# Kernel optimization log

Hardware: AMD Instinct MI355X
Metric: run time of the kernel (lower is better)

Reference implementation:

```python
import jax, jax.numpy as jnp
import numpy as np

NUM_HEADS = 12
HEAD_DIM = 64


def setup_inputs() -> dict:
    key = jax.random.key(0)
    k1, k2, k3 = jax.random.split(key, 3)
    x = jax.random.normal(k1, (64, 768, 14, 14), dtype=jnp.float32)
    # 1x1 conv weights stored as [out_ch, in_ch]; scaled to keep softmax logits sane
    w_qkv = jax.random.normal(k2, (3 * NUM_HEADS * HEAD_DIM, 768), dtype=jnp.float32) * 0.02
    w_proj = jax.random.normal(k3, (768, NUM_HEADS * HEAD_DIM), dtype=jnp.float32) * 0.02
    return {"x": x, "w_qkv": w_qkv, "w_proj": w_proj}


def reference(x, w_qkv, w_proj):
    B, C, H, W = x.shape
    N = H * W
    scale = HEAD_DIM ** -0.25  # qk_scale=None -> head_dim**-0.25, applied to both q and k
    # 1x1 conv == channel matmul: [B,3*nh*dh,H,W]
    qkv = jnp.einsum('oc,bchw->bohw', w_qkv, x)
    # rearrange 'b (x y z) h w -> x b y (h w) z'
    qkv = qkv.reshape(B, 3, NUM_HEADS, HEAD_DIM, N).transpose(1, 0, 2, 4, 3)  # [3,B,nh,N,dh]
    q, k, v = qkv[0], qkv[1], qkv[2]
    attn = jnp.einsum('bhnd,bhmd->bhnm', q * scale, k * scale)  # [B,nh,N,N]
    attn = jax.nn.softmax(attn, axis=-1)
    out = jnp.einsum('bhnm,bhmd->bhnd', attn, v)  # [B,nh,N,dh]
    # rearrange 'b y (h w) z -> b (y z) h w'
    out = out.transpose(0, 1, 3, 2).reshape(B, NUM_HEADS * HEAD_DIM, H, W)
    out = jnp.einsum('oc,bchw->bohw', w_proj, out)  # proj 1x1 conv, no bias
    return out
```

## Files before the change

### kernel.cpp

```cpp
#include <hip/hip_runtime.h>
#include <cstdint>
#include <cstddef>

#define NH     12
#define DH     64
#define CIN    768
#define NPIX   196
#define NB     64
#define ROWS   (NB * NPIX)
#define QKV_OC 2304
#define NKT    12

typedef __attribute__((ext_vector_type(8))) _Float16 f16x8;
typedef __attribute__((ext_vector_type(4))) _Float16 f16x4;
typedef __attribute__((ext_vector_type(4))) float    f32x4;

#define MFMA16 __builtin_amdgcn_mfma_f32_16x16x32_f16

__global__ __launch_bounds__(256) void k_convert_w(const float* __restrict__ wq,
                                                   const float* __restrict__ wp,
                                                   _Float16* __restrict__ out) {
    int i = blockIdx.x * 256 + threadIdx.x;
    const int NQ = QKV_OC * CIN / 4;
    const int NT = NQ + (CIN * CIN) / 4;
    if (i >= NT) return;
    float4 v = (i < NQ) ? ((const float4*)wq)[i] : ((const float4*)wp)[i - NQ];
    f16x4 o = { (_Float16)v.x, (_Float16)v.y, (_Float16)v.z, (_Float16)v.w };
    ((f16x4*)out)[i] = o;
}

__global__ __launch_bounds__(256) void k_transpose_x(const float* __restrict__ x,
                                                     _Float16* __restrict__ Xt) {
    __shared__ __align__(16) _Float16 lds[NPIX][72];
    int t  = threadIdx.x;
    int b  = blockIdx.y, c0 = blockIdx.x * 64;
    const float* xp = x + ((size_t)b * CIN + c0) * NPIX;
    for (int idx = t; idx < 64 * 49; idx += 256) {
        int c = idx / 49, k = idx - c * 49;
        float4 v = *(const float4*)(xp + (size_t)c * NPIX + k * 4);
        int n = k * 4;
        lds[n][c]     = (_Float16)v.x;
        lds[n + 1][c] = (_Float16)v.y;
        lds[n + 2][c] = (_Float16)v.z;
        lds[n + 3][c] = (_Float16)v.w;
    }
    __syncthreads();
    int cs = t & 7, nn = t >> 3;
    for (int n = nn; n < NPIX; n += 32) {
        _Float16* dst = Xt + ((size_t)(b * NPIX + n)) * CIN + c0 + cs * 8;
        *(ulonglong2*)dst = *(const ulonglong2*)&lds[n][cs * 8];
    }
}

__device__ inline void gload16(const _Float16* g, _Float16* l) {
    __builtin_amdgcn_global_load_lds((const __attribute__((address_space(1))) void*)g,
                                     (__attribute__((address_space(3))) void*)l,
                                     16, 0, 0);
}

template<int NTN, bool PROJ>
__global__ __launch_bounds__(512, 2) void k_gemm2(const _Float16* __restrict__ A,
                                                  const _Float16* __restrict__ Bm,
                                                  _Float16* __restrict__ Cb,
                                                  float* __restrict__ Cf) {
    __shared__ __align__(16) _Float16 As[2][256 * 64];
    __shared__ __align__(16) _Float16 Bs[2][256 * 64];
    int tid = threadIdx.x;
    int w = tid >> 6, lane = tid & 63;

    int nwg = gridDim.x;
    int orig = blockIdx.x;
    int q = nwg >> 3, r = nwg & 7;
    int xcd = orig & 7, within = orig >> 3;
    int wg = (xcd < r ? xcd * (q + 1) : r * (q + 1) + (xcd - r) * q) + within;
    int bm = wg / NTN, bn = wg - bm * NTN;
    int m0 = bm * 256, n0 = bn * 256;

    int wr = w >> 2, wc = w & 3;
    int r16 = lane & 15, q4 = lane >> 4;

    int sr8  = (w << 3) + (lane >> 3);
    int swz8 = ((lane & 7) ^ (lane >> 3)) << 3;
    const _Float16* Ag = A  + (size_t)(m0 + sr8) * CIN + swz8;
    const _Float16* Bg = Bm + (size_t)(n0 + sr8) * CIN + swz8;

    auto stageA = [&](int buf, int kt) {
        const _Float16* g = Ag + kt * 64;
        _Float16* l0 = As[buf] + (w << 9);
        gload16(g,             l0);
        gload16(g +  64 * CIN, l0 + 4096);
        gload16(g + 128 * CIN, l0 + 8192);
        gload16(g + 192 * CIN, l0 + 12288);
    };
    auto stageB = [&](int buf, int kt) {
        const _Float16* g = Bg + kt * 64;
        _Float16* l0 = Bs[buf] + (w << 9);
        gload16(g,             l0);
        gload16(g +  64 * CIN, l0 + 4096);
        gload16(g + 128 * CIN, l0 + 8192);
        gload16(g + 192 * CIN, l0 + 12288);
    };

    int cS0 = ((q4)     ^ (r16 & 7)) << 3;
    int cS1 = ((q4 + 4) ^ (r16 & 7)) << 3;

    f32x4 acc[8][4];
#pragma unroll
    for (int i = 0; i < 8; i++)
#pragma unroll
        for (int j = 0; j < 4; j++) acc[i][j] = (f32x4){0.f, 0.f, 0.f, 0.f};

    stageA(0, 0); stageB(0, 0);
    stageA(1, 1); stageB(1, 1);
    asm volatile("s_waitcnt vmcnt(8)" ::: "memory");
    __builtin_amdgcn_sched_barrier(0);
    __builtin_amdgcn_s_barrier();

#pragma unroll 2
    for (int t = 0; t < NKT; ++t) {
        int bt = t & 1;
        const _Float16* Ab = As[bt] + ((wr << 7) + r16) * 64;
        const _Float16* Bb = Bs[bt] + ((wc << 6) + r16) * 64;
        bool pre = (t + 2 < NKT);

        f16x8 a0[4][2], a1[4][2], b0[2][2], b1[2][2];
#pragma unroll
        for (int i = 0; i < 4; i++) {
            a0[i][0] = *(const f16x8*)(Ab + (i << 10) + cS0);
            a0[i][1] = *(const f16x8*)(Ab + (i << 10) + cS1);
            a1[i][0] = *(const f16x8*)(Ab + 4096 + (i << 10) + cS0);
            a1[i][1] = *(const f16x8*)(Ab + 4096 + (i << 10) + cS1);
        }
#pragma unroll
        for (int j = 0; j < 2; j++) {
            b0[j][0] = *(const f16x8*)(Bb + (j << 10) + cS0);
            b0[j][1] = *(const f16x8*)(Bb + (j << 10) + cS1);
            b1[j][0] = *(const f16x8*)(Bb + 2048 + (j << 10) + cS0);
            b1[j][1] = *(const f16x8*)(Bb + 2048 + (j << 10) + cS1);
        }

        __builtin_amdgcn_s_setprio(1);
#pragma unroll
        for (int i = 0; i < 4; i++)
#pragma unroll
            for (int j = 0; j < 2; j++) {
                acc[i][j]     = MFMA16(a0[i][0], b0[j][0], acc[i][j],     0, 0, 0);
                acc[i][j]     = MFMA16(a0[i][1], b0[j][1], acc[i][j],     0, 0, 0);
                acc[4 + i][j] = MFMA16(a1[i][0], b0[j][0], acc[4 + i][j], 0, 0, 0);
                acc[4 + i][j] = MFMA16(a1[i][1], b0[j][1], acc[4 + i][j], 0, 0, 0);
            }
        __builtin_amdgcn_s_setprio(0);

        asm volatile("s_waitcnt lgkmcnt(0)" ::: "memory");
        __builtin_amdgcn_sched_barrier(0);
        __builtin_amdgcn_s_barrier();

        if (pre) { stageA(bt, t + 2); stageB(bt, t + 2); }

        __builtin_amdgcn_s_setprio(1);
#pragma unroll
        for (int i = 0; i < 4; i++)
#pragma unroll
            for (int j = 0; j < 2; j++) {
                acc[i][2 + j]     = MFMA16(a0[i][0], b1[j][0], acc[i][2 + j],     0, 0, 0);
                acc[i][2 + j]     = MFMA16(a0[i][1], b1[j][1], acc[i][2 + j],     0, 0, 0);
                acc[4 + i][2 + j] = MFMA16(a1[i][0], b1[j][0], acc[4 + i][2 + j], 0, 0, 0);
                acc[4 + i][2 + j] = MFMA16(a1[i][1], b1[j][1], acc[4 + i][2 + j], 0, 0, 0);
            }
        __builtin_amdgcn_s_setprio(0);

        if (pre) { asm volatile("s_waitcnt vmcnt(8)" ::: "memory"); }
        else     { asm volatile("s_waitcnt vmcnt(0)" ::: "memory"); }
        __builtin_amdgcn_sched_barrier(0);
        __builtin_amdgcn_s_barrier();
    }

    if (!PROJ) {
#pragma unroll
        for (int hh = 0; hh < 2; hh++)
#pragma unroll
            for (int i = 0; i < 4; i++)
#pragma unroll
                for (int rr = 0; rr < 4; rr++) {
                    int row = m0 + (wr << 7) + hh * 64 + i * 16 + q4 * 4 + rr;
                    _Float16* cp = Cb + (size_t)row * QKV_OC + n0 + (wc << 6) + r16;
#pragma unroll
                    for (int g = 0; g < 2; g++)
#pragma unroll
                        for (int j = 0; j < 2; j++)
                            cp[g * 32 + j * 16] = (_Float16)acc[hh * 4 + i][g * 2 + j][rr];
                }
    } else {
#pragma unroll
        for (int hh = 0; hh < 2; hh++)
#pragma unroll
            for (int i = 0; i < 4; i++) {
                int row = m0 + (wr << 7) + hh * 64 + i * 16 + q4 * 4;
                int b = row / NPIX;
                int n = row - b * NPIX;
#pragma unroll
                for (int g = 0; g < 2; g++)
#pragma unroll
                    for (int j = 0; j < 2; j++) {
                        int col = n0 + (wc << 6) + g * 32 + j * 16 + r16;
                        f32x4 a = acc[hh * 4 + i][g * 2 + j];
                        float4 o; o.x = a[0]; o.y = a[1]; o.z = a[2]; o.w = a[3];
                        *(float4*)(Cf + ((size_t)b * CIN + col) * NPIX + n) = o;
                    }
            }
    }
}

__global__ __launch_bounds__(512) void k_attn(const _Float16* __restrict__ qkv,
                                              _Float16* __restrict__ Ot) {
    __shared__ __align__(16) _Float16 Kl[208 * 64];
    __shared__ __align__(16) _Float16 Vt[64][216];
    __shared__ __align__(16) _Float16 Pl[8][16][216];
    int tid = threadIdx.x, wave = tid >> 6, lane = tid & 63;
    int bh = blockIdx.x;
    int b = bh / NH, h = bh - b * NH;
    const _Float16* base  = qkv + (size_t)b * NPIX * QKV_OC + h * DH;
    const _Float16* kb    = base + CIN;
    const _Float16* vbase = base + 2 * CIN;

    {
        int c8 = lane & 7;
#pragma unroll
        for (int rr = 0; rr < 4; ++rr) {
            int grp = wave + rr * 8;
            if (grp < 26) {
                int row = grp * 8 + (lane >> 3);
                const _Float16* src = kb + (size_t)row * QKV_OC + ((c8 ^ (row & 7)) << 3);
                gload16(src, Kl + row * 64 + (c8 << 3));
            }
        }
    }
    for (int task = tid; task < 208 * 8; task += 512) {
        int m = task >> 3, dc = (task & 7) * 8;
        f16x8 v = *(const f16x8*)(vbase + (size_t)m * QKV_OC + dc);
#pragma unroll
        for (int j = 0; j < 8; j++) Vt[dc + j][m] = v[j];
    }
    __syncthreads();

    int r16 = lane & 15, q4 = lane >> 4, r7 = r16 & 7;
    int kc0 = ((q4)     ^ r7) << 3;
    int kc1 = ((q4 + 4) ^ r7) << 3;
    const float s2 = 0.125f;

    for (int nt = wave; nt < 13; nt += 8) {
        f16x8 aq0 = *(const f16x8*)(base + (size_t)(nt * 16 + r16) * QKV_OC + q4 * 8);
        f16x8 aq1 = *(const f16x8*)(base + (size_t)(nt * 16 + r16) * QKV_OC + 32 + q4 * 8);
        f32x4 L[13];
#pragma unroll
        for (int mt = 0; mt < 13; ++mt) {
            const _Float16* kr = Kl + (mt * 16 + r16) * 64;
            f16x8 bk0 = *(const f16x8*)(kr + kc0);
            f16x8 bk1 = *(const f16x8*)(kr + kc1);
            f32x4 s = {0.f, 0.f, 0.f, 0.f};
            s = MFMA16(aq0, bk0, s, 0, 0, 0);
            s = MFMA16(aq1, bk1, s, 0, 0, 0);
            L[mt] = s;
        }
        float mx[4] = {-1e30f, -1e30f, -1e30f, -1e30f};
#pragma unroll
        for (int mt = 0; mt < 13; ++mt)
#pragma unroll
            for (int r = 0; r < 4; ++r) {
                float lv = L[mt][r] * s2;
                if (mt == 12 && r16 >= 4) lv = -1e30f;
                L[mt][r] = lv;
                mx[r] = fmaxf(mx[r], lv);
            }
#pragma unroll
        for (int r = 0; r < 4; ++r)
            for (int off = 1; off < 16; off <<= 1)
                mx[r] = fmaxf(mx[r], __shfl_xor(mx[r], off));
        float sm[4] = {0.f, 0.f, 0.f, 0.f};
#pragma unroll
        for (int mt = 0; mt < 13; ++mt)
#pragma unroll
            for (int r = 0; r < 4; ++r) {
                float p = exp2f((L[mt][r] - mx[r]) * 1.44269504f);
                sm[r] += p;
                Pl[wave][q4 * 4 + r][mt * 16 + r16] = (_Float16)p;
            }
#pragma unroll
        for (int r = 0; r < 4; ++r)
            for (int off = 1; off < 16; off <<= 1)
                sm[r] += __shfl_xor(sm[r], off);

        f32x4 oacc[4];
#pragma unroll
        for (int di = 0; di < 4; ++di) oacc[di] = (f32x4){0.f, 0.f, 0.f, 0.f};
#pragma unroll
        for (int mc = 0; mc < 6; ++mc) {
            f16x8 ap = *(const f16x8*)&Pl[wave][r16][mc * 32 + q4 * 8];
#pragma unroll
            for (int di = 0; di < 4; ++di) {
                f16x8 bv = *(const f16x8*)&Vt[di * 16 + r16][mc * 32 + q4 * 8];
                oacc[di] = MFMA16(ap, bv, oacc[di], 0, 0, 0);
            }
        }
        {
            _Float16 z = (_Float16)0.f;
            f16x8 zz = (f16x8){z, z, z, z, z, z, z, z};
            f16x8 ap = (q4 < 2) ? *(const f16x8*)&Pl[wave][r16][192 + q4 * 8] : zz;
#pragma unroll
            for (int di = 0; di < 4; ++di) {
                f16x8 bv = (q4 < 2) ? *(const f16x8*)&Vt[di * 16 + r16][192 + q4 * 8] : zz;
                oacc[di] = MFMA16(ap, bv, oacc[di], 0, 0, 0);
            }
        }
#pragma unroll
        for (int r = 0; r < 4; ++r) {
            int n = nt * 16 + q4 * 4 + r;
            if (n < NPIX) {
                float rinv = 1.0f / sm[r];
                _Float16* op = Ot + (size_t)(b * NPIX + n) * CIN + h * DH + r16;
#pragma unroll
                for (int di = 0; di < 4; ++di)
                    op[di * 16] = (_Float16)(oacc[di][r] * rinv);
            }
        }
    }
}

extern "C" void kernel_launch(void* const* d_in, const int* in_sizes, int n_in,
                              void* d_out, int out_size, void* d_ws, size_t ws_size,
                              hipStream_t stream) {
    const float* x  = (const float*)d_in[0];
    const float* wq = (const float*)d_in[1];
    const float* wp = (const float*)d_in[2];
    float* out = (float*)d_out;
    char* ws = (char*)d_ws;

    _Float16* Xt  = (_Float16*)(ws);
    _Float16* W   = (_Float16*)(ws + 20447232);
    _Float16* qkv = (_Float16*)(ws + 25165824);
    _Float16* Ot  = (_Float16*)(ws + 86507520);
    _Float16* Wq = W;
    _Float16* Wp = W + (size_t)QKV_OC * CIN;

    hipLaunchKernelGGL(k_convert_w, dim3(2304), dim3(256), 0, stream, wq, wp, W);
    hipLaunchKernelGGL(k_transpose_x, dim3(12, 64), dim3(256), 0, stream, x, Xt);
    hipLaunchKernelGGL((k_gemm2<9, false>), dim3(49 * 9), dim3(512), 0, stream,
                       Xt, Wq, qkv, (float*)nullptr);
    hipLaunchKernelGGL(k_attn, dim3(768), dim3(512), 0, stream, qkv, Ot);
    hipLaunchKernelGGL((k_gemm2<3, true>), dim3(49 * 3), dim3(512), 0, stream,
                       Ot, Wp, (_Float16*)nullptr, out);
}
```

Measured before the change: 137.1 us.

## Load GEMM B operand directly from global into registers, dropping LDS staging

The B tile no longer goes through a double-buffered LDS stage. Each wave now reads its B fragments straight from global memory into registers at every k-step, and only A keeps the global-to-LDS prefetch, so the vmcnt thresholds are halved. This removes half the LDS traffic and halves shared memory per block, which may let two blocks fit per CU. The cost is unprefetched global-latency loads on the critical path, duplicate B reads across waves in the same column, and possible compiler-inserted waits that also stall on the outstanding A prefetch.

```diff
diff --git a/kernel.cpp b/kernel.cpp
--- a/kernel.cpp
+++ b/kernel.cpp
@@ -64,7 +64,6 @@
                                                   _Float16* __restrict__ Cb,
                                                   float* __restrict__ Cf) {
     __shared__ __align__(16) _Float16 As[2][256 * 64];
-    __shared__ __align__(16) _Float16 Bs[2][256 * 64];
     int tid = threadIdx.x;
     int w = tid >> 6, lane = tid & 63;
 
@@ -81,8 +80,7 @@
 
     int sr8  = (w << 3) + (lane >> 3);
     int swz8 = ((lane & 7) ^ (lane >> 3)) << 3;
-    const _Float16* Ag = A  + (size_t)(m0 + sr8) * CIN + swz8;
-    const _Float16* Bg = Bm + (size_t)(n0 + sr8) * CIN + swz8;
+    const _Float16* Ag = A + (size_t)(m0 + sr8) * CIN + swz8;
 
     auto stageA = [&](int buf, int kt) {
         const _Float16* g = Ag + kt * 64;
@@ -92,14 +90,8 @@
         gload16(g + 128 * CIN, l0 + 8192);
         gload16(g + 192 * CIN, l0 + 12288);
     };
-    auto stageB = [&](int buf, int kt) {
-        const _Float16* g = Bg + kt * 64;
-        _Float16* l0 = Bs[buf] + (w << 9);
-        gload16(g,             l0);
-        gload16(g +  64 * CIN, l0 + 4096);
-        gload16(g + 128 * CIN, l0 + 8192);
-        gload16(g + 192 * CIN, l0 + 12288);
-    };
+
+    const _Float16* Bg = Bm + (size_t)(n0 + (wc << 6) + r16) * CIN + (q4 << 3);
 
     int cS0 = ((q4)     ^ (r16 & 7)) << 3;
     int cS1 = ((q4 + 4) ^ (r16 & 7)) << 3;
@@ -110,9 +102,8 @@
 #pragma unroll
         for (int j = 0; j < 4; j++) acc[i][j] = (f32x4){0.f, 0.f, 0.f, 0.f};
 
-    stageA(0, 0); stageB(0, 0);
-    stageA(1, 1); stageB(1, 1);
-    asm volatile("s_waitcnt vmcnt(8)" ::: "memory");
+    stageA(0, 0); stageA(1, 1);
+    asm volatile("s_waitcnt vmcnt(4)" ::: "memory");
     __builtin_amdgcn_sched_barrier(0);
     __builtin_amdgcn_s_barrier();
 
@@ -120,10 +111,16 @@
     for (int t = 0; t < NKT; ++t) {
         int bt = t & 1;
         const _Float16* Ab = As[bt] + ((wr << 7) + r16) * 64;
-        const _Float16* Bb = Bs[bt] + ((wc << 6) + r16) * 64;
         bool pre = (t + 2 < NKT);
 
-        f16x8 a0[4][2], a1[4][2], b0[2][2], b1[2][2];
+        f16x8 bf[4][2];
+#pragma unroll
+        for (int jj = 0; jj < 4; jj++)
+#pragma unroll
+            for (int h = 0; h < 2; h++)
+                bf[jj][h] = *(const f16x8*)(Bg + (size_t)jj * 16 * CIN + t * 64 + h * 32);
+
+        f16x8 a0[4][2], a1[4][2];
 #pragma unroll
         for (int i = 0; i < 4; i++) {
             a0[i][0] = *(const f16x8*)(Ab + (i << 10) + cS0);
@@ -131,23 +128,16 @@
             a1[i][0] = *(const f16x8*)(Ab + 4096 + (i << 10) + cS0);
             a1[i][1] = *(const f16x8*)(Ab + 4096 + (i << 10) + cS1);
         }
-#pragma unroll
-        for (int j = 0; j < 2; j++) {
-            b0[j][0] = *(const f16x8*)(Bb + (j << 10) + cS0);
-            b0[j][1] = *(const f16x8*)(Bb + (j << 10) + cS1);
-            b1[j][0] = *(const f16x8*)(Bb + 2048 + (j << 10) + cS0);
-            b1[j][1] = *(const f16x8*)(Bb + 2048 + (j << 10) + cS1);
-        }
 
         __builtin_amdgcn_s_setprio(1);
 #pragma unroll
         for (int i = 0; i < 4; i++)
 #pragma unroll
             for (int j = 0; j < 2; j++) {
-                acc[i][j]     = MFMA16(a0[i][0], b0[j][0], acc[i][j],     0, 0, 0);
-                acc[i][j]     = MFMA16(a0[i][1], b0[j][1], acc[i][j],     0, 0, 0);
-                acc[4 + i][j] = MFMA16(a1[i][0], b0[j][0], acc[4 + i][j], 0, 0, 0);
-                acc[4 + i][j] = MFMA16(a1[i][1], b0[j][1], acc[4 + i][j], 0, 0, 0);
+                acc[i][j]     = MFMA16(a0[i][0], bf[j][0], acc[i][j],     0, 0, 0);
+                acc[i][j]     = MFMA16(a0[i][1], bf[j][1], acc[i][j],     0, 0, 0);
+                acc[4 + i][j] = MFMA16(a1[i][0], bf[j][0], acc[4 + i][j], 0, 0, 0);
+                acc[4 + i][j] = MFMA16(a1[i][1], bf[j][1], acc[4 + i][j], 0, 0, 0);
             }
         __builtin_amdgcn_s_setprio(0);
 
@@ -155,21 +145,21 @@
         __builtin_amdgcn_sched_barrier(0);
         __builtin_amdgcn_s_barrier();
 
-        if (pre) { stageA(bt, t + 2); stageB(bt, t + 2); }
+        if (pre) stageA(bt, t + 2);
 
         __builtin_amdgcn_s_setprio(1);
 #pragma unroll
         for (int i = 0; i < 4; i++)
 #pragma unroll
             for (int j = 0; j < 2; j++) {
-                acc[i][2 + j]     = MFMA16(a0[i][0], b1[j][0], acc[i][2 + j],     0, 0, 0);
-                acc[i][2 + j]     = MFMA16(a0[i][1], b1[j][1], acc[i][2 + j],     0, 0, 0);
-                acc[4 + i][2 + j] = MFMA16(a1[i][0], b1[j][0], acc[4 + i][2 + j], 0, 0, 0);
-                acc[4 + i][2 + j] = MFMA16(a1[i][1], b1[j][1], acc[4 + i][2 + j], 0, 0, 0);
+                acc[i][2 + j]     = MFMA16(a0[i][0], bf[2 + j][0], acc[i][2 + j],     0, 0, 0);
+                acc[i][2 + j]     = MFMA16(a0[i][1], bf[2 + j][1], acc[i][2 + j],     0, 0, 0);
+                acc[4 + i][2 + j] = MFMA16(a1[i][0], bf[2 + j][0], acc[4 + i][2 + j], 0, 0, 0);
+                acc[4 + i][2 + j] = MFMA16(a1[i][1], bf[2 + j][1], acc[4 + i][2 + j], 0, 0, 0);
             }
         __builtin_amdgcn_s_setprio(0);
 
-        if (pre) { asm volatile("s_waitcnt vmcnt(8)" ::: "memory"); }
+        if (pre) { asm volatile("s_waitcnt vmcnt(4)" ::: "memory"); }
         else     { asm volatile("s_waitcnt vmcnt(0)" ::: "memory"); }
         __builtin_amdgcn_sched_barrier(0);
         __builtin_amdgcn_s_barrier();
```

Measured after the change: 186.4 us. 1.36x slower.
